# Performance work log

Measured on AMD Instinct MI355X. Metric: run time of the kernel, lower is better.

Reference implementation:

```python
import jax, jax.numpy as jnp
import numpy as np

B, C, H, W = 8, 256, 64, 64

def setup_inputs() -> dict:
    key = jax.random.key(0)
    ks = jax.random.split(key, 8)
    s = 0.02  # keep logits in a sane range
    return {
        "x": jax.random.normal(ks[0], (B, C, H, W), jnp.float32),
        "motion_info": jax.random.normal(ks[1], (B, C, H, W), jnp.float32),
        "wq": jax.random.normal(ks[2], (C, C), jnp.float32) * s,
        "bq": jax.random.normal(ks[3], (C,), jnp.float32) * s,
        "wk": jax.random.normal(ks[4], (C, C), jnp.float32) * s,
        "bk": jax.random.normal(ks[5], (C,), jnp.float32) * s,
        "wv": jax.random.normal(ks[6], (C, C), jnp.float32) * s,
        "bv": jax.random.normal(ks[7], (C,), jnp.float32) * s,
    }

def reference(x, motion_info, wq, bq, wk, bk, wv, bv):
    b, c, h, w = x.shape
    n = h * w
    scale = c ** (-0.5)
    # 1x1 convs == channel-mixing GEMMs; flatten spatial to tokens
    xf = x.reshape(b, c, n)              # [B,C,N]
    mf = motion_info.reshape(b, c, n)    # [B,C,N]
    q = jnp.einsum('dc,bcn->bdn', wq, xf) + bq[None, :, None]
    k = jnp.einsum('dc,bcn->bdn', wk, mf) + bk[None, :, None]
    v = jnp.einsum('dc,bcn->bdn', wv, mf) + bv[None, :, None]
    # attn[b,i,j] = <q[:,i], k[:,j]> * scale, softmax over j
    attn = jax.nn.softmax(jnp.einsum('bci,bcj->bij', q, k) * scale, axis=-1)
    # out[b,c,i] = sum_j v[b,c,j] * attn[b,i,j]
    out = jnp.einsum('bcj,bij->bci', v, attn)
    return out.reshape(b, c, h, w)
```

## Files before the change

### kernel.cpp

```cpp
#include <hip/hip_runtime.h>
#include <hip/hip_bf16.h>

#define BATCH 8
#define CH    256
#define NTOK  4096

typedef __bf16 bf16_t;
typedef __bf16 bf16x8 __attribute__((ext_vector_type(8)));
typedef __bf16 bf16x4 __attribute__((ext_vector_type(4)));
typedef float  fx4    __attribute__((ext_vector_type(4)));


__global__ __launch_bounds__(256, 2) void proj_kernel(
    const float* __restrict__ x, const float* __restrict__ motion,
    const float* __restrict__ wq, const float* __restrict__ bq,
    const float* __restrict__ wk, const float* __restrict__ bk,
    const float* __restrict__ wv, const float* __restrict__ bv,
    bf16_t* __restrict__ qg, bf16_t* __restrict__ kg, bf16_t* __restrict__ vg)
{
    const int mat = blockIdx.y;
    const int b   = blockIdx.x & 7;
    const int n0  = (blockIdx.x >> 3) * 64;
    const float* __restrict__ src  = (mat == 0) ? x  : motion;
    const float* __restrict__ W    = (mat == 0) ? wq : (mat == 1 ? wk : wv);
    const float* __restrict__ bias = (mat == 0) ? bq : (mat == 1 ? bk : bv);

    __shared__ __align__(16) unsigned char smem[55296 + 1024];
    bf16_t* Xt    = (bf16_t*)smem;
    bf16_t* Wl    = (bf16_t*)(smem + 33792);
    bf16_t* OutL  = (bf16_t*)smem;
    float*  biasL = (float*)(smem + 55296);

    const int tid  = threadIdx.x;
    const int w    = tid >> 6;
    const int lane = tid & 63;
    const int l16  = lane & 15;
    const int quad = lane >> 4;

    biasL[tid] = bias[tid];

    for (int it = 0; it < 16; ++it) {
        const int c  = it * 16 + (tid >> 4);
        const int j4 = (tid & 15) * 4;
        const float4 v = *(const float4*)&src[((size_t)b * CH + c) * NTOK + n0 + j4];
        Xt[(j4 + 0) * 264 + c] = (bf16_t)v.x;
        Xt[(j4 + 1) * 264 + c] = (bf16_t)v.y;
        Xt[(j4 + 2) * 264 + c] = (bf16_t)v.z;
        Xt[(j4 + 3) * 264 + c] = (bf16_t)v.w;
    }

    fx4 acc[16];
    for (int i = 0; i < 16; ++i) acc[i] = (fx4){0.f, 0.f, 0.f, 0.f};

    for (int cs = 0; cs < 8; ++cs) {
        for (int it = 0; it < 8; ++it) {
            const int d  = it * 32 + (tid >> 3);
            const int c4 = (tid & 7) * 4;
            const float4 v = *(const float4*)&W[(size_t)d * CH + cs * 32 + c4];
            bf16x4 pk;
            pk[0] = (bf16_t)v.x; pk[1] = (bf16_t)v.y;
            pk[2] = (bf16_t)v.z; pk[3] = (bf16_t)v.w;
            *(bf16x4*)&Wl[d * 40 + c4] = pk;
        }
        __syncthreads();
        const bf16x8 af = *(const bf16x8*)&Xt[(w * 16 + l16) * 264 + cs * 32 + quad * 8];
        for (int dp = 0; dp < 16; ++dp) {
            const bf16x8 bf = *(const bf16x8*)&Wl[(dp * 16 + l16) * 40 + quad * 8];
            acc[dp] = __builtin_amdgcn_mfma_f32_16x16x32_bf16(af, bf, acc[dp], 0, 0, 0);
        }
        __syncthreads();
    }

    const float qs = (mat == 0) ? 0.0625f : 1.0f;
    for (int dp = 0; dp < 16; ++dp) {
        const int d = dp * 16 + l16;
        const float bb = biasL[d];
        bf16x4 pk;
        for (int r = 0; r < 4; ++r)
            pk[r] = (bf16_t)((acc[dp][r] + bb) * qs);
        *(bf16x4*)&OutL[d * 72 + w * 16 + quad * 4] = pk;
    }
    __syncthreads();

    if (mat < 2) {
        bf16_t* __restrict__ G = (mat == 0) ? qg : kg;
        for (int it = 0; it < 8; ++it) {
            const int n  = it * 8 + (tid >> 5);
            const int d8 = (tid & 31) * 8;
            bf16x8 vv;
            for (int k = 0; k < 8; ++k) vv[k] = OutL[(d8 + k) * 72 + n];
            *(bf16x8*)&G[((size_t)b * NTOK + n0 + n) * CH + d8] = vv;
        }
    } else {
        for (int it = 0; it < 8; ++it) {
            const int d  = it * 32 + (tid >> 3);
            const int n8 = (tid & 7) * 8;
            const bf16x8 vv = *(const bf16x8*)&OutL[d * 72 + n8];
            *(bf16x8*)&vg[((size_t)b * CH + d) * NTOK + n0 + n8] = vv;
        }
    }
}

__global__ __launch_bounds__(256, 3) void attn_kernel(
    const bf16_t* __restrict__ qg, const bf16_t* __restrict__ kg,
    const bf16_t* __restrict__ vg, float* __restrict__ out)
{
    const int b  = blockIdx.x & 7;
    const int i0 = (blockIdx.x >> 3) * 64;

    __shared__ __align__(16) unsigned char smem[42752];
    bf16_t* Kt   = (bf16_t*)smem;
    bf16_t* Vt   = (bf16_t*)(smem + 16896);
    bf16_t* Pb   = (bf16_t*)(smem + 37376);
    float*  lred = (float*)(smem + 42496);

    const int tid = threadIdx.x;
    const int w = tid >> 6, lane = tid & 63, l16 = lane & 15, quad = lane >> 4;

    bf16x8 qf[8];
    {
        const bf16_t* qb = qg + ((size_t)b * NTOK + i0 + w * 16 + l16) * CH;
        for (int cs = 0; cs < 8; ++cs)
            qf[cs] = *(const bf16x8*)&qb[cs * 32 + quad * 8];
    }

    fx4 oacc[16];
    for (int i = 0; i < 16; ++i) oacc[i] = (fx4){0.f, 0.f, 0.f, 0.f};
    float rs[4] = {0.f, 0.f, 0.f, 0.f};

    bf16_t* PbW = Pb + w * (16 * 40);

    for (int jt = 0; jt < 128; ++jt) {
        const int j0 = jt * 32;
        for (int it = 0; it < 4; ++it) {
            const int j  = it * 8 + (tid >> 5);
            const int c8 = (tid & 31) * 8;
            *(bf16x8*)&Kt[j * 264 + c8] =
                *(const bf16x8*)&kg[((size_t)b * NTOK + j0 + j) * CH + c8];
        }
        for (int it = 0; it < 4; ++it) {
            const int c  = it * 64 + (tid >> 2);
            const int j8 = (tid & 3) * 8;
            *(bf16x8*)&Vt[c * 40 + j8] =
                *(const bf16x8*)&vg[((size_t)b * CH + c) * NTOK + j0 + j8];
        }
        __syncthreads();

        for (int jp = 0; jp < 2; ++jp) {
            fx4 s = (fx4){0.f, 0.f, 0.f, 0.f};
            for (int cs = 0; cs < 8; ++cs) {
                const bf16x8 kf =
                    *(const bf16x8*)&Kt[(jp * 16 + l16) * 264 + cs * 32 + quad * 8];
                s = __builtin_amdgcn_mfma_f32_16x16x32_bf16(qf[cs], kf, s, 0, 0, 0);
            }
            for (int r = 0; r < 4; ++r) {
                const float p = __expf(s[r]);
                rs[r] += p;
                PbW[(quad * 4 + r) * 40 + jp * 16 + l16] = (bf16_t)p;
            }
        }
        __syncthreads();

        const bf16x8 pf = *(const bf16x8*)&PbW[l16 * 40 + quad * 8];
        for (int cp = 0; cp < 16; ++cp) {
            const bf16x8 vf = *(const bf16x8*)&Vt[(cp * 16 + l16) * 40 + quad * 8];
            oacc[cp] = __builtin_amdgcn_mfma_f32_16x16x32_bf16(vf, pf, oacc[cp], 0, 0, 0);
        }
        __syncthreads();
    }

    for (int r = 0; r < 4; ++r) {
        float v = rs[r];
        v += __shfl_xor(v, 1);
        v += __shfl_xor(v, 2);
        v += __shfl_xor(v, 4);
        v += __shfl_xor(v, 8);
        rs[r] = v;
    }
    if (l16 == 0)
        for (int r = 0; r < 4; ++r) lred[w * 16 + quad * 4 + r] = rs[r];
    __syncthreads();
    const float linv = 1.0f / lred[w * 16 + l16];

    const int i = i0 + w * 16 + l16;
    for (int cp = 0; cp < 16; ++cp) {
        for (int r = 0; r < 4; ++r) {
            const int c = cp * 16 + quad * 4 + r;
            out[((size_t)b * CH + c) * NTOK + i] = oacc[cp][r] * linv;
        }
    }
}

extern "C" void kernel_launch(void* const* d_in, const int* in_sizes, int n_in,
                              void* d_out, int out_size, void* d_ws, size_t ws_size,
                              hipStream_t stream) {
    const float* x  = (const float*)d_in[0];
    const float* mi = (const float*)d_in[1];
    const float* wq = (const float*)d_in[2];
    const float* bq = (const float*)d_in[3];
    const float* wk = (const float*)d_in[4];
    const float* bk = (const float*)d_in[5];
    const float* wv = (const float*)d_in[6];
    const float* bv = (const float*)d_in[7];

    bf16_t* qg = (bf16_t*)d_ws;
    bf16_t* kg = qg + (size_t)BATCH * NTOK * CH;
    bf16_t* vg = kg + (size_t)BATCH * NTOK * CH;

    dim3 pgrid(BATCH * (NTOK / 64), 3);
    proj_kernel<<<pgrid, 256, 0, stream>>>(x, mi, wq, bq, wk, bk, wv, bv, qg, kg, vg);
    attn_kernel<<<BATCH * (NTOK / 64), 256, 0, stream>>>(qg, kg, vg, (float*)d_out);
}
```

Measured before the change: 395.4 us.

## Switch to 32x32 MFMA tiles, pre-convert weights, split keys across waves

Both kernels now use 32x32x16 bf16 MFMA instead of 16x16x32. A separate kernel converts the weights to bf16 once per call, parking them in the output buffer as scratch so the projection reads bf16 weights straight from global memory without per-tile LDS staging. Attention tiles grow to 64 keys per iteration, with each wave pair splitting the key range and merging partial outputs through LDS at the end. Each wave writes and reads its own P buffer, so one block barrier per iteration is replaced by an lgkmcnt wait. The row sums now come from the bf16-rounded P values. Larger LDS use lowers attention occupancy to two blocks per CU.

```diff
diff --git a/kernel.cpp b/kernel.cpp
--- a/kernel.cpp
+++ b/kernel.cpp
@@ -8,186 +8,214 @@
 typedef __bf16 bf16_t;
 typedef __bf16 bf16x8 __attribute__((ext_vector_type(8)));
 typedef __bf16 bf16x4 __attribute__((ext_vector_type(4)));
-typedef float  fx4    __attribute__((ext_vector_type(4)));
-
-
-__global__ __launch_bounds__(256, 2) void proj_kernel(
+typedef float  fx16   __attribute__((ext_vector_type(16)));
+
+
+__global__ void wcvt_kernel(const float* __restrict__ wq, const float* __restrict__ wk,
+                            const float* __restrict__ wv, bf16_t* __restrict__ wb) {
+    const int idx = (blockIdx.x * 256 + threadIdx.x) * 4;
+    const int mat = idx >> 16;
+    const int off = idx & 65535;
+    const float* src = (mat == 0) ? wq : (mat == 1 ? wk : wv);
+    const float4 v = *(const float4*)&src[off];
+    bf16x4 o;
+    o[0] = (bf16_t)v.x; o[1] = (bf16_t)v.y; o[2] = (bf16_t)v.z; o[3] = (bf16_t)v.w;
+    *(bf16x4*)&wb[idx] = o;
+}
+
+__global__ __launch_bounds__(256, 4) void proj_kernel(
     const float* __restrict__ x, const float* __restrict__ motion,
-    const float* __restrict__ wq, const float* __restrict__ bq,
-    const float* __restrict__ wk, const float* __restrict__ bk,
-    const float* __restrict__ wv, const float* __restrict__ bv,
+    const bf16_t* __restrict__ wb,
+    const float* __restrict__ bq, const float* __restrict__ bk, const float* __restrict__ bv,
     bf16_t* __restrict__ qg, bf16_t* __restrict__ kg, bf16_t* __restrict__ vg)
 {
     const int mat = blockIdx.y;
     const int b   = blockIdx.x & 7;
     const int n0  = (blockIdx.x >> 3) * 64;
-    const float* __restrict__ src  = (mat == 0) ? x  : motion;
-    const float* __restrict__ W    = (mat == 0) ? wq : (mat == 1 ? wk : wv);
-    const float* __restrict__ bias = (mat == 0) ? bq : (mat == 1 ? bk : bv);
-
-    __shared__ __align__(16) unsigned char smem[55296 + 1024];
+    const float*  __restrict__ src  = (mat == 0) ? x : motion;
+    const bf16_t* __restrict__ W    = wb + mat * 65536;
+    const float*  __restrict__ bias = (mat == 0) ? bq : (mat == 1 ? bk : bv);
+
+    __shared__ __align__(16) unsigned char smem[36864];
     bf16_t* Xt    = (bf16_t*)smem;
-    bf16_t* Wl    = (bf16_t*)(smem + 33792);
     bf16_t* OutL  = (bf16_t*)smem;
-    float*  biasL = (float*)(smem + 55296);
 
     const int tid  = threadIdx.x;
     const int w    = tid >> 6;
     const int lane = tid & 63;
-    const int l16  = lane & 15;
-    const int quad = lane >> 4;
-
-    biasL[tid] = bias[tid];
-
-    for (int it = 0; it < 16; ++it) {
-        const int c  = it * 16 + (tid >> 4);
-        const int j4 = (tid & 15) * 4;
-        const float4 v = *(const float4*)&src[((size_t)b * CH + c) * NTOK + n0 + j4];
-        Xt[(j4 + 0) * 264 + c] = (bf16_t)v.x;
-        Xt[(j4 + 1) * 264 + c] = (bf16_t)v.y;
-        Xt[(j4 + 2) * 264 + c] = (bf16_t)v.z;
-        Xt[(j4 + 3) * 264 + c] = (bf16_t)v.w;
-    }
-
-    fx4 acc[16];
-    for (int i = 0; i < 16; ++i) acc[i] = (fx4){0.f, 0.f, 0.f, 0.f};
-
-    for (int cs = 0; cs < 8; ++cs) {
+    const int l32  = lane & 31;
+    const int half = lane >> 5;
+    const int s    = w & 1;
+    const int dh   = w >> 1;
+
+    {
+        const int n  = tid & 63;
+        const int cg = tid >> 6;
         for (int it = 0; it < 8; ++it) {
-            const int d  = it * 32 + (tid >> 3);
-            const int c4 = (tid & 7) * 4;
-            const float4 v = *(const float4*)&W[(size_t)d * CH + cs * 32 + c4];
-            bf16x4 pk;
-            pk[0] = (bf16_t)v.x; pk[1] = (bf16_t)v.y;
-            pk[2] = (bf16_t)v.z; pk[3] = (bf16_t)v.w;
-            *(bf16x4*)&Wl[d * 40 + c4] = pk;
-        }
-        __syncthreads();
-        const bf16x8 af = *(const bf16x8*)&Xt[(w * 16 + l16) * 264 + cs * 32 + quad * 8];
-        for (int dp = 0; dp < 16; ++dp) {
-            const bf16x8 bf = *(const bf16x8*)&Wl[(dp * 16 + l16) * 40 + quad * 8];
-            acc[dp] = __builtin_amdgcn_mfma_f32_16x16x32_bf16(af, bf, acc[dp], 0, 0, 0);
-        }
-        __syncthreads();
-    }
+            const int c0 = it * 32 + cg * 8;
+            bf16x8 pk;
+            for (int k = 0; k < 8; ++k)
+                pk[k] = (bf16_t)src[((size_t)b * CH + c0 + k) * NTOK + n0 + n];
+            *(bf16x8*)&Xt[n * 264 + c0] = pk;
+        }
+    }
+    __syncthreads();
+
+    fx16 acc[4];
+    for (int dp = 0; dp < 4; ++dp)
+        for (int r = 0; r < 16; ++r) acc[dp][r] = 0.f;
+
+    for (int ks = 0; ks < 16; ++ks) {
+        const bf16x8 af = *(const bf16x8*)&Xt[(s * 32 + l32) * 264 + ks * 16 + half * 8];
+        for (int dp = 0; dp < 4; ++dp) {
+            const int d = dh * 128 + dp * 32 + l32;
+            const bf16x8 wf = *(const bf16x8*)&W[d * 256 + ks * 16 + half * 8];
+            acc[dp] = __builtin_amdgcn_mfma_f32_32x32x16_bf16(af, wf, acc[dp], 0, 0, 0);
+        }
+    }
+    __syncthreads();
 
     const float qs = (mat == 0) ? 0.0625f : 1.0f;
-    for (int dp = 0; dp < 16; ++dp) {
-        const int d = dp * 16 + l16;
-        const float bb = biasL[d];
-        bf16x4 pk;
-        for (int r = 0; r < 4; ++r)
-            pk[r] = (bf16_t)((acc[dp][r] + bb) * qs);
-        *(bf16x4*)&OutL[d * 72 + w * 16 + quad * 4] = pk;
-    }
-    __syncthreads();
 
     if (mat < 2) {
+        for (int dp = 0; dp < 4; ++dp) {
+            const int d = dh * 128 + dp * 32 + l32;
+            const float bb = bias[d];
+            for (int r = 0; r < 16; ++r) {
+                const int n = s * 32 + (r & 3) + 8 * (r >> 2) + 4 * half;
+                OutL[n * 264 + d] = (bf16_t)((acc[dp][r] + bb) * qs);
+            }
+        }
+        __syncthreads();
         bf16_t* __restrict__ G = (mat == 0) ? qg : kg;
-        for (int it = 0; it < 8; ++it) {
-            const int n  = it * 8 + (tid >> 5);
-            const int d8 = (tid & 31) * 8;
-            bf16x8 vv;
-            for (int k = 0; k < 8; ++k) vv[k] = OutL[(d8 + k) * 72 + n];
-            *(bf16x8*)&G[((size_t)b * NTOK + n0 + n) * CH + d8] = vv;
+        for (int it = 0; it < 2; ++it) {
+            const int n  = it * 32 + (tid >> 3);
+            const int db = (tid & 7) * 32;
+            for (int u = 0; u < 4; ++u)
+                *(bf16x8*)&G[((size_t)b * NTOK + n0 + n) * CH + db + u * 8] =
+                    *(const bf16x8*)&OutL[n * 264 + db + u * 8];
         }
     } else {
-        for (int it = 0; it < 8; ++it) {
-            const int d  = it * 32 + (tid >> 3);
-            const int n8 = (tid & 7) * 8;
-            const bf16x8 vv = *(const bf16x8*)&OutL[d * 72 + n8];
-            *(bf16x8*)&vg[((size_t)b * CH + d) * NTOK + n0 + n8] = vv;
-        }
-    }
-}
-
-__global__ __launch_bounds__(256, 3) void attn_kernel(
+        bf16_t* OutLv = (bf16_t*)smem;
+        for (int dp = 0; dp < 4; ++dp) {
+            const int d = dh * 128 + dp * 32 + l32;
+            const float bb = bias[d];
+            for (int r = 0; r < 16; ++r) {
+                const int n = s * 32 + (r & 3) + 8 * (r >> 2) + 4 * half;
+                OutLv[d * 72 + n] = (bf16_t)(acc[dp][r] + bb);
+            }
+        }
+        __syncthreads();
+        for (int it = 0; it < 2; ++it) {
+            const int d  = it * 128 + (tid >> 1);
+            const int nb = (tid & 1) * 32;
+            for (int u = 0; u < 4; ++u)
+                *(bf16x8*)&vg[((size_t)b * CH + d) * NTOK + n0 + nb + u * 8] =
+                    *(const bf16x8*)&OutLv[d * 72 + nb + u * 8];
+        }
+    }
+}
+
+__global__ __launch_bounds__(256, 2) void attn_kernel(
     const bf16_t* __restrict__ qg, const bf16_t* __restrict__ kg,
     const bf16_t* __restrict__ vg, float* __restrict__ out)
 {
     const int b  = blockIdx.x & 7;
     const int i0 = (blockIdx.x >> 3) * 64;
 
-    __shared__ __align__(16) unsigned char smem[42752];
+    __shared__ __align__(16) unsigned char smem[81408];
     bf16_t* Kt   = (bf16_t*)smem;
-    bf16_t* Vt   = (bf16_t*)(smem + 16896);
-    bf16_t* Pb   = (bf16_t*)(smem + 37376);
-    float*  lred = (float*)(smem + 42496);
-
-    const int tid = threadIdx.x;
-    const int w = tid >> 6, lane = tid & 63, l16 = lane & 15, quad = lane >> 4;
-
-    bf16x8 qf[8];
+    bf16_t* Vt   = (bf16_t*)(smem + 33792);
+    bf16_t* Pw   = (bf16_t*)(smem + 70656);
+    float*  lred = (float*)(smem + 80896);
+
+    const int tid  = threadIdx.x;
+    const int w    = tid >> 6;
+    const int lane = tid & 63;
+    const int l32  = lane & 31;
+    const int half = lane >> 5;
+    const int s    = w & 1;
+    const int h    = w >> 1;
+
+    bf16x8 qf[16];
     {
-        const bf16_t* qb = qg + ((size_t)b * NTOK + i0 + w * 16 + l16) * CH;
-        for (int cs = 0; cs < 8; ++cs)
-            qf[cs] = *(const bf16x8*)&qb[cs * 32 + quad * 8];
-    }
-
-    fx4 oacc[16];
-    for (int i = 0; i < 16; ++i) oacc[i] = (fx4){0.f, 0.f, 0.f, 0.f};
-    float rs[4] = {0.f, 0.f, 0.f, 0.f};
-
-    bf16_t* PbW = Pb + w * (16 * 40);
-
-    for (int jt = 0; jt < 128; ++jt) {
-        const int j0 = jt * 32;
-        for (int it = 0; it < 4; ++it) {
+        const bf16_t* qrow = qg + ((size_t)b * NTOK + i0 + s * 32 + l32) * CH;
+        for (int ks = 0; ks < 16; ++ks)
+            qf[ks] = *(const bf16x8*)&qrow[ks * 16 + half * 8];
+    }
+
+    fx16 oacc[8];
+    for (int cp = 0; cp < 8; ++cp)
+        for (int r = 0; r < 16; ++r) oacc[cp][r] = 0.f;
+    float rs = 0.f;
+
+    bf16_t* Pme = Pw + w * 1280;
+
+    for (int jt = 0; jt < 64; ++jt) {
+        const int j0 = jt * 64;
+        for (int it = 0; it < 8; ++it) {
             const int j  = it * 8 + (tid >> 5);
-            const int c8 = (tid & 31) * 8;
-            *(bf16x8*)&Kt[j * 264 + c8] =
-                *(const bf16x8*)&kg[((size_t)b * NTOK + j0 + j) * CH + c8];
-        }
-        for (int it = 0; it < 4; ++it) {
-            const int c  = it * 64 + (tid >> 2);
-            const int j8 = (tid & 3) * 8;
-            *(bf16x8*)&Vt[c * 40 + j8] =
-                *(const bf16x8*)&vg[((size_t)b * CH + c) * NTOK + j0 + j8];
-        }
-        __syncthreads();
-
-        for (int jp = 0; jp < 2; ++jp) {
-            fx4 s = (fx4){0.f, 0.f, 0.f, 0.f};
-            for (int cs = 0; cs < 8; ++cs) {
-                const bf16x8 kf =
-                    *(const bf16x8*)&Kt[(jp * 16 + l16) * 264 + cs * 32 + quad * 8];
-                s = __builtin_amdgcn_mfma_f32_16x16x32_bf16(qf[cs], kf, s, 0, 0, 0);
-            }
-            for (int r = 0; r < 4; ++r) {
-                const float p = __expf(s[r]);
-                rs[r] += p;
-                PbW[(quad * 4 + r) * 40 + jp * 16 + l16] = (bf16_t)p;
-            }
-        }
-        __syncthreads();
-
-        const bf16x8 pf = *(const bf16x8*)&PbW[l16 * 40 + quad * 8];
-        for (int cp = 0; cp < 16; ++cp) {
-            const bf16x8 vf = *(const bf16x8*)&Vt[(cp * 16 + l16) * 40 + quad * 8];
-            oacc[cp] = __builtin_amdgcn_mfma_f32_16x16x32_bf16(vf, pf, oacc[cp], 0, 0, 0);
-        }
-        __syncthreads();
-    }
-
-    for (int r = 0; r < 4; ++r) {
-        float v = rs[r];
-        v += __shfl_xor(v, 1);
-        v += __shfl_xor(v, 2);
-        v += __shfl_xor(v, 4);
-        v += __shfl_xor(v, 8);
-        rs[r] = v;
-    }
-    if (l16 == 0)
-        for (int r = 0; r < 4; ++r) lred[w * 16 + quad * 4 + r] = rs[r];
+            const int ch = (tid & 31) * 8;
+            *(bf16x8*)&Kt[j * 264 + ch] =
+                *(const bf16x8*)&kg[((size_t)b * NTOK + j0 + j) * CH + ch];
+        }
+        for (int it = 0; it < 8; ++it) {
+            const int c  = it * 32 + (tid >> 3);
+            const int ch = (tid & 7) * 8;
+            *(bf16x8*)&Vt[c * 72 + ch] =
+                *(const bf16x8*)&vg[((size_t)b * CH + c) * NTOK + j0 + ch];
+        }
+        __syncthreads();
+
+        fx16 sacc;
+        for (int r = 0; r < 16; ++r) sacc[r] = 0.f;
+        for (int ks = 0; ks < 16; ++ks) {
+            const bf16x8 kf =
+                *(const bf16x8*)&Kt[(h * 32 + l32) * 264 + ks * 16 + half * 8];
+            sacc = __builtin_amdgcn_mfma_f32_32x32x16_bf16(qf[ks], kf, sacc, 0, 0, 0);
+        }
+
+        for (int r = 0; r < 16; ++r) {
+            const float p = __expf(sacc[r]);
+            const int row = (r & 3) + 8 * (r >> 2) + 4 * half;
+            Pme[row * 40 + l32] = (bf16_t)p;
+        }
+        __asm__ volatile("s_waitcnt lgkmcnt(0)" ::: "memory");
+
+        for (int ks2 = 0; ks2 < 2; ++ks2) {
+            const bf16x8 pf = *(const bf16x8*)&Pme[l32 * 40 + ks2 * 16 + half * 8];
+            for (int k = 0; k < 8; ++k) rs += (float)pf[k];
+            for (int cp = 0; cp < 8; ++cp) {
+                const bf16x8 vf =
+                    *(const bf16x8*)&Vt[(cp * 32 + l32) * 72 + h * 32 + ks2 * 16 + half * 8];
+                oacc[cp] = __builtin_amdgcn_mfma_f32_32x32x16_bf16(vf, pf, oacc[cp], 0, 0, 0);
+            }
+        }
+        __syncthreads();
+    }
+
+    rs += __shfl_xor(rs, 32);
+    if (half == 0) lred[(s * 2 + h) * 32 + l32] = rs;
+
+    float* scr = (float*)smem;
+    if (h == 1) {
+        for (int cp = 0; cp < 8; ++cp)
+            for (int r = 0; r < 16; ++r) {
+                const int c = cp * 32 + (r & 3) + 8 * (r >> 2) + 4 * half;
+                scr[((size_t)s * 256 + c) * 32 + l32] = oacc[cp][r];
+            }
+    }
     __syncthreads();
-    const float linv = 1.0f / lred[w * 16 + l16];
-
-    const int i = i0 + w * 16 + l16;
-    for (int cp = 0; cp < 16; ++cp) {
-        for (int r = 0; r < 4; ++r) {
-            const int c = cp * 16 + quad * 4 + r;
-            out[((size_t)b * CH + c) * NTOK + i] = oacc[cp][r] * linv;
-        }
+    if (h == 0) {
+        const float linv = 1.0f / (lred[(s * 2 + 0) * 32 + l32] +
+                                   lred[(s * 2 + 1) * 32 + l32]);
+        const int i = i0 + s * 32 + l32;
+        for (int cp = 0; cp < 8; ++cp)
+            for (int r = 0; r < 16; ++r) {
+                const int c = cp * 32 + (r & 3) + 8 * (r >> 2) + 4 * half;
+                out[((size_t)b * CH + c) * NTOK + i] =
+                    (oacc[cp][r] + scr[((size_t)s * 256 + c) * 32 + l32]) * linv;
+            }
     }
 }
 
@@ -206,8 +234,10 @@
     bf16_t* qg = (bf16_t*)d_ws;
     bf16_t* kg = qg + (size_t)BATCH * NTOK * CH;
     bf16_t* vg = kg + (size_t)BATCH * NTOK * CH;
-
+    bf16_t* wb = (bf16_t*)d_out;
+
+    wcvt_kernel<<<192, 256, 0, stream>>>(wq, wk, wv, wb);
     dim3 pgrid(BATCH * (NTOK / 64), 3);
-    proj_kernel<<<pgrid, 256, 0, stream>>>(x, mi, wq, bq, wk, bk, wv, bv, qg, kg, vg);
+    proj_kernel<<<pgrid, 256, 0, stream>>>(x, mi, wb, bq, bk, bv, qg, kg, vg);
     attn_kernel<<<BATCH * (NTOK / 64), 256, 0, stream>>>(qg, kg, vg, (float*)d_out);
 }
```

Result: slower. 547.3 us (+38.4%).
